# Performance work log

Measured on AMD Instinct MI355X. Metric: run time of the kernel, lower is better.

## Reference

```python
import jax, jax.numpy as jnp
import numpy as np
import math

N = 100000
D = 128       # input_dim
DK = 32       # d_k
H = 4         # heads
DV = D // H   # d_v = 32
DFF = 512     # 4 * input_dim
EPS = 1e-5


def layer_norm(x, g, b):
    mu = jnp.mean(x, axis=-1, keepdims=True)
    var = jnp.var(x, axis=-1, keepdims=True)
    return (x - mu) * jax.lax.rsqrt(var + EPS) * g + b


def setup_inputs() -> dict:
    key = jax.random.key(0)
    ks = jax.random.split(key, 10)
    x = jax.random.normal(ks[0], (N, D), dtype=jnp.float32)
    neighbor_index = jax.random.randint(ks[1], (N, 4), 0, N)
    # xavier-ish scaled params
    w_q = jax.random.normal(ks[2], (H, D, DK), dtype=jnp.float32) * math.sqrt(2.0 / (D + DK))
    w_k = jax.random.normal(ks[3], (H, 5, D, DK), dtype=jnp.float32) * math.sqrt(2.0 / (D + DK))
    w_v = jax.random.normal(ks[4], (H, 5, D, DV), dtype=jnp.float32) * math.sqrt(2.0 / (D + DV))
    W1 = jax.random.normal(ks[5], (D, DFF), dtype=jnp.float32) * math.sqrt(1.0 / D)
    b1 = jnp.zeros((DFF,), dtype=jnp.float32)
    W2 = jax.random.normal(ks[6], (DFF, D), dtype=jnp.float32) * math.sqrt(1.0 / DFF)
    b2 = jnp.zeros((D,), dtype=jnp.float32)
    g1 = jnp.ones((D,), dtype=jnp.float32)
    beta1 = jnp.zeros((D,), dtype=jnp.float32)
    g2 = jnp.ones((D,), dtype=jnp.float32)
    beta2 = jnp.zeros((D,), dtype=jnp.float32)
    return {"x": x, "neighbor_index": neighbor_index, "w_q": w_q, "w_k": w_k,
            "w_v": w_v, "W1": W1, "b1": b1, "W2": W2, "b2": b2,
            "g1": g1, "beta1": beta1, "g2": g2, "beta2": beta2}


def attention(x, neighbor_index, w_q, w_k, w_v):
    # gather the 4 typed neighbors and prepend the self node -> (N, 5, D)
    x_nb = jnp.concatenate([x[:, None, :], x[neighbor_index]], axis=1)
    Q = jnp.einsum('nd,hdk->hnk', x, w_q)                 # (H, N, DK)
    K = jnp.einsum('nrd,hrdk->hnrk', x_nb, w_k)           # (H, N, 5, DK)
    V = jnp.einsum('nrd,hrdv->hnrv', x_nb, w_v)           # (H, N, 5, DV)
    A = jnp.einsum('hnk,hnrk->hnr', Q, K) / math.sqrt(DK)
    # NOTE: original torch code applies softmax over dim=1 (the node axis),
    # reproduced faithfully here.
    A = jax.nn.softmax(A, axis=1)
    Z = jnp.einsum('hnr,hnrv->hnv', A, V)                 # (H, N, DV)
    return jnp.transpose(Z, (1, 0, 2)).reshape(x.shape[0], -1)  # (N, H*DV)


def reference(x, neighbor_index, w_q, w_k, w_v, W1, b1, W2, b2, g1, beta1, g2, beta2):
    attn = attention(x, neighbor_index, w_q, w_k, w_v)
    h = layer_norm(x + attn, g1, beta1)
    ffn = jax.nn.relu(h @ W1 + b1) @ W2 + b2
    return layer_norm(h + ffn, g2, beta2)
```

## Files before the change

kernel.cpp:

```cpp
#include <hip/hip_runtime.h>
#include <hip/hip_bf16.h>

typedef unsigned short u16;
typedef __attribute__((ext_vector_type(8))) short short8;
typedef __attribute__((ext_vector_type(4))) float f32x4;
typedef __attribute__((ext_vector_type(4))) float float4v;
typedef __attribute__((ext_vector_type(4))) unsigned short us4;
typedef __attribute__((ext_vector_type(2))) unsigned int uint2v;

#define NN       100000
#define OFF_WK   16384
#define OFF_WV   98304
#define OFF_W1   180224
#define PACK_ELEMS 311296

#define WS_LWS   0u
#define WS_PM    8000000u
#define WS_PS    8000640u
#define WS_MHR   8001280u
#define WS_ISHR  8001408u
#define WS_PK    8001536u
#define WS_XB    8624128u
#define WS_SV    34224128u

#define PWS_PITCH 36
#define PWS_SLICE 1280

static __device__ __forceinline__ float b2f(u16 u){
  unsigned int i = ((unsigned int)u) << 16;
  float f; __builtin_memcpy(&f, &i, 4); return f;
}
static __device__ __forceinline__ u16 f2b(float f){
  unsigned int i; __builtin_memcpy(&i, &f, 4);
  i += 0x7FFFu + ((i >> 16) & 1u);
  return (u16)(i >> 16);
}
static __device__ __forceinline__ f32x4 mfma16(short8 a, short8 b, f32x4 c){
  return __builtin_amdgcn_mfma_f32_16x16x32_bf16(a, b, c, 0, 0, 0);
}
static __device__ __forceinline__ bool detect32(const void* g1){
  return ((const u16*)g1)[0] == 0;
}
static __device__ __forceinline__ float ldf(const void* p, size_t i, bool is32){
  return is32 ? ((const float*)p)[i] : b2f(((const u16*)p)[i]);
}
static __device__ __forceinline__ short8 lds_afrag(const u16* p){
  uint2v a = *(const uint2v*)p;
  uint2v b = *(const uint2v*)(p + 4);
  short8 r;
  unsigned int* rp = (unsigned int*)&r;
  rp[0] = a.x; rp[1] = a.y; rp[2] = b.x; rp[3] = b.y;
  return r;
}

__global__ __launch_bounds__(256) void k_convert_x(
    const void* __restrict__ x, const void* __restrict__ g1, u16* __restrict__ xb)
{
  const bool is32 = detect32(g1);
  size_t i = (size_t)blockIdx.x * 256 + threadIdx.x;
  us4 o;
  if (is32){
    float4v v = ((const float4v*)x)[i];
    o.x = f2b(v.x); o.y = f2b(v.y); o.z = f2b(v.z); o.w = f2b(v.w);
  } else {
    o = ((const us4*)x)[i];
  }
  ((us4*)xb)[i] = o;
}

__global__ __launch_bounds__(256) void k_convert_small(
    const void* b1, const void* b2, const void* g1, const void* be1,
    const void* g2, const void* be2, u16* __restrict__ sv)
{
  const bool is32 = detect32(g1);
  for (int i = threadIdx.x; i < 1152; i += 256){
    const void* src; int off;
    if      (i < 512) { src = b1;  off = i; }
    else if (i < 640) { src = b2;  off = i - 512; }
    else if (i < 768) { src = g1;  off = i - 640; }
    else if (i < 896) { src = be1; off = i - 768; }
    else if (i < 1024){ src = g2;  off = i - 896; }
    else              { src = be2; off = i - 1024; }
    sv[i] = f2b(ldf(src, off, is32));
  }
}

__global__ __launch_bounds__(256) void k_pack(
    const void* __restrict__ wq, const void* __restrict__ wk,
    const void* __restrict__ wv, const void* __restrict__ W1,
    const void* __restrict__ W2, const void* __restrict__ g1,
    u16* __restrict__ pk)
{
  const bool is32 = detect32(g1);
  int p = blockIdx.x * 256 + threadIdx.x;
  if (p >= PACK_ELEMS) return;
  float v;
  if (p < OFF_WK){
    int q = p;
    int j = q & 7, lane = (q >> 3) & 63, tk = q >> 9;
    int kb = tk & 3, t = tk >> 2;
    int kd = kb*32 + (lane>>4)*8 + j, nc = t*16 + (lane & 15);
    v = ldf(wq, (size_t)(nc>>5)*4096 + kd*32 + (nc & 31), is32);
  } else if (p < OFF_WV){
    int q = p - OFF_WK; int r = q >> 14; q &= 16383;
    int j = q & 7, lane = (q >> 3) & 63, tk = q >> 9;
    int kb = tk & 3, t = tk >> 2;
    int kd = kb*32 + (lane>>4)*8 + j, nc = t*16 + (lane & 15);
    v = ldf(wk, (size_t)((nc>>5)*5 + r)*4096 + kd*32 + (nc & 31), is32);
  } else if (p < OFF_W1){
    int q = p - OFF_WV; int r = q >> 14; q &= 16383;
    int j = q & 7, lane = (q >> 3) & 63, tk = q >> 9;
    int kb = tk & 3, t = tk >> 2;
    int kd = kb*32 + (lane>>4)*8 + j, nc = t*16 + (lane & 15);
    v = ldf(wv, (size_t)((nc>>5)*5 + r)*4096 + kd*32 + (nc & 31), is32);
  } else {
    int q = p - OFF_W1;
    int j = q & 7, lane = (q >> 3) & 63, rest = q >> 9;
    int pairIdx = rest >> 4, sub = rest & 15;
    int c = pairIdx >> 2, kb2 = pairIdx & 3;
    int half = lane >> 4, mc = lane & 15;
    if (sub < 8){
      int u = sub >> 2, kb = sub & 3;
      int kd = kb*32 + half*8 + j;
      int nc = c*128 + (kb2*2+u)*16 + mc;
      v = ldf(W1, (size_t)kd*512 + nc, is32);
    } else {
      int t = sub - 8;
      int kd = (c*4+kb2)*32 + half*8 + j;
      int nc = t*16 + mc;
      v = ldf(W2, (size_t)kd*128 + nc, is32);
    }
  }
  pk[p] = f2b(v);
}

__global__ __launch_bounds__(256, 3) void k_qk(
    const u16* __restrict__ x, const int* __restrict__ nbr,
    const u16* __restrict__ pw, float* __restrict__ lws)
{
  __shared__ __align__(16) u16 sbuf[16384];
  const int tid = threadIdx.x, lane = tid & 63, wv = tid >> 6;
  const int m = lane & 15, quad = lane >> 4;
  const int n0 = blockIdx.x * 128 + wv * 32;
  const bool act0 = (n0 < NN), act1 = (n0 + 16 < NN);

  const short8* sb8 = (const short8*)sbuf;
  for (int s = tid; s < 2048; s += 256)
    ((short8*)sbuf)[s] = ((const short8*)pw)[s];
  __syncthreads();

  short8 a[2][4];
  f32x4 q[2][8];
  #pragma unroll
  for (int tl = 0; tl < 2; tl++)
    #pragma unroll
    for (int t = 0; t < 8; t++) q[tl][t] = (f32x4){0.f,0.f,0.f,0.f};

  #pragma unroll
  for (int tl = 0; tl < 2; tl++){
    if (!(tl ? act1 : act0)) continue;
    const short8* xp = (const short8*)(x + (size_t)(n0 + tl*16 + m) * 128);
    #pragma unroll
    for (int kb = 0; kb < 4; kb++) a[tl][kb] = xp[kb*4 + quad];
  }
  #pragma unroll
  for (int t = 0; t < 8; t++){
    short8 bfr[4];
    #pragma unroll
    for (int kb = 0; kb < 4; kb++) bfr[kb] = sb8[(t*4+kb)*64 + lane];
    #pragma unroll
    for (int tl = 0; tl < 2; tl++){
      if (!(tl ? act1 : act0)) continue;
      #pragma unroll
      for (int kb = 0; kb < 4; kb++) q[tl][t] = mfma16(a[tl][kb], bfr[kb], q[tl][t]);
    }
  }

  for (int r = 0; r < 5; r++){
    __syncthreads();
    for (int s = tid; s < 2048; s += 256)
      ((short8*)sbuf)[s] = ((const short8*)(pw + OFF_WK + (size_t)r*16384))[s];
    __syncthreads();
    if (r > 0){
      #pragma unroll
      for (int tl = 0; tl < 2; tl++){
        if (!(tl ? act1 : act0)) continue;
        int node = nbr[(size_t)(n0 + tl*16 + m)*4 + (r-1)];
        const short8* xp = (const short8*)(x + (size_t)node * 128);
        #pragma unroll
        for (int kb = 0; kb < 4; kb++) a[tl][kb] = xp[kb*4 + quad];
      }
    }
    #pragma unroll
    for (int h = 0; h < 4; h++){
      short8 b0[4], b1f[4];
      #pragma unroll
      for (int kb = 0; kb < 4; kb++){
        b0[kb]  = sb8[((2*h  )*4+kb)*64 + lane];
        b1f[kb] = sb8[((2*h+1)*4+kb)*64 + lane];
      }
      #pragma unroll
      for (int tl = 0; tl < 2; tl++){
        if (!(tl ? act1 : act0)) continue;
        f32x4 k0 = {0.f,0.f,0.f,0.f}, k1 = {0.f,0.f,0.f,0.f};
        #pragma unroll
        for (int kb = 0; kb < 4; kb++){
          k0 = mfma16(a[tl][kb], b0[kb],  k0);
          k1 = mfma16(a[tl][kb], b1f[kb], k1);
        }
        float p[4];
        #pragma unroll
        for (int i = 0; i < 4; i++) p[i] = q[tl][2*h][i]*k0[i] + q[tl][2*h+1][i]*k1[i];
        #pragma unroll
        for (int mask = 1; mask < 16; mask <<= 1){
          #pragma unroll
          for (int i = 0; i < 4; i++) p[i] += __shfl_xor(p[i], mask, 16);
        }
        if (m == 0){
          #pragma unroll
          for (int i = 0; i < 4; i++)
            lws[(size_t)(h*5+r)*NN + n0 + tl*16 + quad*4 + i]
                = p[i] * 0.17677669529663687f;
        }
      }
    }
  }
}

__global__ __launch_bounds__(256) void k_red_part(
    const float* __restrict__ lws, float* __restrict__ pm, float* __restrict__ ps)
{
  const int hr = blockIdx.x >> 3, pb = blockIdx.x & 7;
  const int start = pb * 12500, end = start + 12500;
  const float* v = lws + (size_t)hr * NN;
  __shared__ float red[256];
  float mx = -1e30f;
  for (int i = start + threadIdx.x; i < end; i += 256) mx = fmaxf(mx, v[i]);
  red[threadIdx.x] = mx; __syncthreads();
  for (int s = 128; s > 0; s >>= 1){
    if ((int)threadIdx.x < s) red[threadIdx.x] = fmaxf(red[threadIdx.x], red[threadIdx.x+s]);
    __syncthreads();
  }
  mx = red[0]; __syncthreads();
  float sm = 0.f;
  for (int i = start + threadIdx.x; i < end; i += 256) sm += __expf(v[i] - mx);
  red[threadIdx.x] = sm; __syncthreads();
  for (int s = 128; s > 0; s >>= 1){
    if ((int)threadIdx.x < s) red[threadIdx.x] += red[threadIdx.x+s];
    __syncthreads();
  }
  if (threadIdx.x == 0){ pm[blockIdx.x] = mx; ps[blockIdx.x] = red[0]; }
}

__global__ __launch_bounds__(64) void k_red_fin(
    const float* __restrict__ pm, const float* __restrict__ ps,
    float* __restrict__ mhr, float* __restrict__ ishr)
{
  int t = threadIdx.x;
  if (t < 20){
    float M = -1e30f;
    for (int b = 0; b < 8; b++) M = fmaxf(M, pm[t*8+b]);
    float S = 0.f;
    for (int b = 0; b < 8; b++) S += ps[t*8+b] * __expf(pm[t*8+b] - M);
    mhr[t] = M; ishr[t] = 1.0f / S;
  }
}

__global__ __launch_bounds__(256, 3) void k_attn_ffn(
    const u16* __restrict__ x, const void* __restrict__ xraw,
    const int* __restrict__ nbr,
    const u16* __restrict__ pw, const float* __restrict__ lws,
    const float* __restrict__ mhr, const float* __restrict__ ishr,
    const u16* __restrict__ sv, const void* __restrict__ g1raw,
    float* __restrict__ out)
{
  __shared__ __align__(16) u16 sbuf[16384];
  __shared__ __align__(16) u16 upool[5120];
  const int tid = threadIdx.x, lane = tid & 63, wv = tid >> 6;
  const int m = lane & 15, quad = lane >> 4;
  const int n0 = blockIdx.x * 128 + wv * 32;
  const bool act0 = (n0 < NN), act1 = (n0 + 16 < NN);
  const bool is32 = detect32(g1raw);
  const u16* b1s = sv;
  const u16* b2s = sv + 512;
  const u16* g1s = sv + 640;
  const u16* be1s = sv + 768;
  const u16* g2s = sv + 896;
  const u16* be2s = sv + 1024;
  const short8* sb8 = (const short8*)sbuf;
  float* attw_w = ((float*)upool) + wv * 640;
  u16*   pws_w  = upool + wv * PWS_SLICE;

  for (int j = lane; j < 640; j += 64){
    int tl = j / 320, rem = j - tl*320;
    int r = rem >> 6, h = (rem >> 4) & 3, mm = rem & 15, hr = h*5 + r;
    int node = n0 + tl*16 + mm;
    attw_w[j] = (node < NN)
        ? __expf(lws[(size_t)hr*NN + node] - mhr[hr]) * ishr[hr] : 0.f;
  }

  f32x4 zacc[2][8];
  #pragma unroll
  for (int tl = 0; tl < 2; tl++)
    #pragma unroll
    for (int t = 0; t < 8; t++) zacc[tl][t] = (f32x4){0.f,0.f,0.f,0.f};

  short8 a2[2][4];
  for (int r = 0; r < 5; r++){
    __syncthreads();
    for (int s = tid; s < 2048; s += 256)
      ((short8*)sbuf)[s] = ((const short8*)(pw + OFF_WV + (size_t)r*16384))[s];
    __syncthreads();

    #pragma unroll
    for (int tl = 0; tl < 2; tl++){
      if (!(tl ? act1 : act0)) continue;
      int rowb = n0 + tl*16;
      const short8* xp;
      if (r == 0) xp = (const short8*)(x + (size_t)(rowb + m) * 128);
      else {
        int node = nbr[(size_t)(rowb + m)*4 + (r-1)];
        xp = (const short8*)(x + (size_t)node * 128);
      }
      #pragma unroll
      for (int kb = 0; kb < 4; kb++) a2[tl][kb] = xp[kb*4 + quad];
    }
    #pragma unroll
    for (int t = 0; t < 8; t++){
      short8 bfr[4];
      #pragma unroll
      for (int kb = 0; kb < 4; kb++) bfr[kb] = sb8[(t*4+kb)*64 + lane];
      int h = t >> 1;
      #pragma unroll
      for (int tl = 0; tl < 2; tl++){
        if (!(tl ? act1 : act0)) continue;
        f32x4 v = {0.f,0.f,0.f,0.f};
        #pragma unroll
        for (int kb = 0; kb < 4; kb++) v = mfma16(a2[tl][kb], bfr[kb], v);
        const float* aw = attw_w + tl*320 + (r*4+h)*16;
        #pragma unroll
        for (int i = 0; i < 4; i++) zacc[tl][t][i] += aw[quad*4+i] * v[i];
      }
    }
  }

  float mu[2][4], rs[2][4];
  #pragma unroll
  for (int tl = 0; tl < 2; tl++){
    if (!(tl ? act1 : act0)) continue;
    int rowb = n0 + tl*16;
    #pragma unroll
    for (int t = 0; t < 8; t++)
      #pragma unroll
      for (int i = 0; i < 4; i++)
        zacc[tl][t][i] += ldf(xraw, (size_t)(rowb + quad*4 + i)*128 + t*16 + m, is32);
    float s1[4] = {0,0,0,0}, s2[4] = {0,0,0,0};
    #pragma unroll
    for (int t = 0; t < 8; t++)
      #pragma unroll
      for (int i = 0; i < 4; i++){ float y = zacc[tl][t][i]; s1[i] += y; s2[i] += y*y; }
    #pragma unroll
    for (int mask = 1; mask < 16; mask <<= 1){
      #pragma unroll
      for (int i = 0; i < 4; i++){
        s1[i] += __shfl_xor(s1[i], mask, 16);
        s2[i] += __shfl_xor(s2[i], mask, 16);
      }
    }
    #pragma unroll
    for (int i = 0; i < 4; i++){
      mu[tl][i] = s1[i] * (1.f/128.f);
      float var = s2[i] * (1.f/128.f) - mu[tl][i]*mu[tl][i];
      rs[tl][i] = rsqrtf(var + 1e-5f);
    }
  }

  unsigned int hDp[2][8][2];
  short8 ah[2][4];
  #pragma unroll
  for (int kb = 0; kb < 4; kb++){
    #pragma unroll
    for (int u = 0; u < 2; u++){
      int t = kb*2 + u;
      #pragma unroll
      for (int tl = 0; tl < 2; tl++){
        if (!(tl ? act1 : act0)) continue;
        float gg = b2f(g1s[t*16+m]), bb = b2f(be1s[t*16+m]);
        u16 hv[4];
        #pragma unroll
        for (int i = 0; i < 4; i++){
          hv[i] = f2b((zacc[tl][t][i]-mu[tl][i])*rs[tl][i]*gg + bb);
          pws_w[(tl*16 + quad*4 + i)*PWS_PITCH + u*16 + m] = hv[i];
        }
        hDp[tl][t][0] = (unsigned int)hv[0] | ((unsigned int)hv[1] << 16);
        hDp[tl][t][1] = (unsigned int)hv[2] | ((unsigned int)hv[3] << 16);
      }
    }
    #pragma unroll
    for (int tl = 0; tl < 2; tl++)
      ah[tl][kb] = lds_afrag(pws_w + (tl*16 + m)*PWS_PITCH + quad*8);
  }

  f32x4 f2acc[2][8];
  #pragma unroll
  for (int tl = 0; tl < 2; tl++)
    #pragma unroll
    for (int t = 0; t < 8; t++) f2acc[tl][t] = (f32x4){0.f,0.f,0.f,0.f};

  for (int c = 0; c < 4; c++){
    for (int kp = 0; kp < 2; kp++){
      __syncthreads();
      for (int s = tid; s < 2048; s += 256)
        ((short8*)sbuf)[s] =
            ((const short8*)(pw + OFF_W1 + (size_t)(c*4 + kp*2)*8192))[s];
      __syncthreads();
      #pragma unroll
      for (int kb2w = 0; kb2w < 2; kb2w++){
        int kb2 = kp*2 + kb2w;
        const short8* w1f = sb8 + kb2w*1024;
        const short8* w2f = w1f + 512;
        #pragma unroll
        for (int u = 0; u < 2; u++){
          short8 bfr[4];
          #pragma unroll
          for (int kb = 0; kb < 4; kb++) bfr[kb] = w1f[(u*4+kb)*64 + lane];
          float b1c = b2f(b1s[c*128 + (kb2*2+u)*16 + m]);
          #pragma unroll
          for (int tl = 0; tl < 2; tl++){
            if (!(tl ? act1 : act0)) continue;
            f32x4 g = {0.f,0.f,0.f,0.f};
            #pragma unroll
            for (int kb = 0; kb < 4; kb++) g = mfma16(ah[tl][kb], bfr[kb], g);
            #pragma unroll
            for (int i = 0; i < 4; i++)
              pws_w[(tl*16 + quad*4 + i)*PWS_PITCH + u*16 + m]
                  = f2b(fmaxf(g[i] + b1c, 0.f));
          }
        }
        short8 ag[2];
        #pragma unroll
        for (int tl = 0; tl < 2; tl++)
          ag[tl] = lds_afrag(pws_w + (tl*16 + m)*PWS_PITCH + quad*8);
        #pragma unroll
        for (int t = 0; t < 8; t++){
          short8 bf = w2f[t*64 + lane];
          #pragma unroll
          for (int tl = 0; tl < 2; tl++){
            if (!(tl ? act1 : act0)) continue;
            f2acc[tl][t] = mfma16(ag[tl], bf, f2acc[tl][t]);
          }
        }
      }
    }
  }

  #pragma unroll
  for (int tl = 0; tl < 2; tl++){
    if (!(tl ? act1 : act0)) continue;
    int rowb = n0 + tl*16;
    #pragma unroll
    for (int t = 0; t < 8; t++){
      float b2c = b2f(b2s[t*16 + m]);
      f2acc[tl][t][0] += b2f((u16)(hDp[tl][t][0] & 0xffff)) + b2c;
      f2acc[tl][t][1] += b2f((u16)(hDp[tl][t][0] >> 16))    + b2c;
      f2acc[tl][t][2] += b2f((u16)(hDp[tl][t][1] & 0xffff)) + b2c;
      f2acc[tl][t][3] += b2f((u16)(hDp[tl][t][1] >> 16))    + b2c;
    }
    float s1[4] = {0,0,0,0}, s2[4] = {0,0,0,0};
    #pragma unroll
    for (int t = 0; t < 8; t++)
      #pragma unroll
      for (int i = 0; i < 4; i++){ float y = f2acc[tl][t][i]; s1[i] += y; s2[i] += y*y; }
    #pragma unroll
    for (int mask = 1; mask < 16; mask <<= 1){
      #pragma unroll
      for (int i = 0; i < 4; i++){
        s1[i] += __shfl_xor(s1[i], mask, 16);
        s2[i] += __shfl_xor(s2[i], mask, 16);
      }
    }
    float mu2[4], rs2[4];
    #pragma unroll
    for (int i = 0; i < 4; i++){
      mu2[i] = s1[i] * (1.f/128.f);
      float var = s2[i] * (1.f/128.f) - mu2[i]*mu2[i];
      rs2[i] = rsqrtf(var + 1e-5f);
    }
    #pragma unroll
    for (int t = 0; t < 8; t++){
      float gg = b2f(g2s[t*16+m]), bb = b2f(be2s[t*16+m]);
      #pragma unroll
      for (int i = 0; i < 4; i++)
        out[(size_t)(rowb + quad*4 + i)*128 + t*16 + m] =
            (f2acc[tl][t][i]-mu2[i])*rs2[i]*gg + bb;
    }
  }
}

extern "C" void kernel_launch(void* const* d_in, const int* in_sizes, int n_in,
                              void* d_out, int out_size, void* d_ws, size_t ws_size,
                              hipStream_t stream)
{
  const void* x   = d_in[0];
  const int*  nbr = (const int*)d_in[1];
  const void* wq  = d_in[2];
  const void* wk  = d_in[3];
  const void* wv  = d_in[4];
  const void* W1  = d_in[5];
  const void* b1  = d_in[6];
  const void* W2  = d_in[7];
  const void* b2  = d_in[8];
  const void* g1  = d_in[9];
  const void* be1 = d_in[10];
  const void* g2  = d_in[11];
  const void* be2 = d_in[12];
  float* out = (float*)d_out;

  char* ws = (char*)d_ws;
  float* lws  = (float*)(ws + WS_LWS);
  float* pm   = (float*)(ws + WS_PM);
  float* ps   = (float*)(ws + WS_PS);
  float* mhr  = (float*)(ws + WS_MHR);
  float* ishr = (float*)(ws + WS_ISHR);
  u16*   pk   = (u16*)  (ws + WS_PK);
  u16*   xb   = (u16*)  (ws + WS_XB);
  u16*   sv   = (u16*)  (ws + WS_SV);

  k_convert_x<<<dim3(12500), dim3(256), 0, stream>>>(x, g1, xb);
  k_convert_small<<<dim3(1), dim3(256), 0, stream>>>(b1, b2, g1, be1, g2, be2, sv);
  k_pack<<<dim3((PACK_ELEMS+255)/256), dim3(256), 0, stream>>>(wq, wk, wv, W1, W2, g1, pk);
  k_qk<<<dim3((NN+127)/128), dim3(256), 0, stream>>>(xb, nbr, pk, lws);
  k_red_part<<<dim3(160), dim3(256), 0, stream>>>(lws, pm, ps);
  k_red_fin<<<dim3(1), dim3(64), 0, stream>>>(pm, ps, mhr, ishr);
  k_attn_ffn<<<dim3((NN+127)/128), dim3(256), 0, stream>>>(xb, x, nbr, pk, lws, mhr, ishr,
                                                           sv, g1, out);
}
```

Before: 353.1 us.

## Double-buffer weight tiles in LDS with register prefetch and gather prefetch

Both main kernels now stage weight tiles through a double-buffered LDS area. The next tile and the next neighbor-row gather are loaded into registers while the current tile's MFMAs run, which cuts the two barriers per stage down to one and hides global load latency. Neighbor indices are fetched once as a vector load, and the LDS pitch becomes 40 so A-fragments can be read with a single 16-byte load. The cost is twice the LDS and extra registers, so occupancy falls from 3 to 2 blocks per CU.

```diff
diff --git a/kernel.cpp b/kernel.cpp
--- a/kernel.cpp
+++ b/kernel.cpp
@@ -6,7 +6,7 @@
 typedef __attribute__((ext_vector_type(4))) float f32x4;
 typedef __attribute__((ext_vector_type(4))) float float4v;
 typedef __attribute__((ext_vector_type(4))) unsigned short us4;
-typedef __attribute__((ext_vector_type(2))) unsigned int uint2v;
+typedef __attribute__((ext_vector_type(4))) int int4v;
 
 #define NN       100000
 #define OFF_WK   16384
@@ -23,7 +23,7 @@
 #define WS_XB    8624128u
 #define WS_SV    34224128u
 
-#define PWS_PITCH 36
+#define PWS_PITCH 40
 #define PWS_SLICE 1280
 
 static __device__ __forceinline__ float b2f(u16 u){
@@ -43,14 +43,6 @@
 }
 static __device__ __forceinline__ float ldf(const void* p, size_t i, bool is32){
   return is32 ? ((const float*)p)[i] : b2f(((const u16*)p)[i]);
-}
-static __device__ __forceinline__ short8 lds_afrag(const u16* p){
-  uint2v a = *(const uint2v*)p;
-  uint2v b = *(const uint2v*)(p + 4);
-  short8 r;
-  unsigned int* rp = (unsigned int*)&r;
-  rp[0] = a.x; rp[1] = a.y; rp[2] = b.x; rp[3] = b.y;
-  return r;
 }
 
 __global__ __launch_bounds__(256) void k_convert_x(
@@ -134,61 +126,75 @@
   pk[p] = f2b(v);
 }
 
-__global__ __launch_bounds__(256, 3) void k_qk(
+__global__ __launch_bounds__(256, 2) void k_qk(
     const u16* __restrict__ x, const int* __restrict__ nbr,
     const u16* __restrict__ pw, float* __restrict__ lws)
 {
-  __shared__ __align__(16) u16 sbuf[16384];
+  __shared__ __align__(16) u16 sbuf[32768];
   const int tid = threadIdx.x, lane = tid & 63, wv = tid >> 6;
   const int m = lane & 15, quad = lane >> 4;
   const int n0 = blockIdx.x * 128 + wv * 32;
   const bool act0 = (n0 < NN), act1 = (n0 + 16 < NN);
-
-  const short8* sb8 = (const short8*)sbuf;
-  for (int s = tid; s < 2048; s += 256)
-    ((short8*)sbuf)[s] = ((const short8*)pw)[s];
-  __syncthreads();
-
-  short8 a[2][4];
-  f32x4 q[2][8];
-  #pragma unroll
-  for (int tl = 0; tl < 2; tl++)
-    #pragma unroll
-    for (int t = 0; t < 8; t++) q[tl][t] = (f32x4){0.f,0.f,0.f,0.f};
-
+  short8* sb = (short8*)sbuf;
+  const short8* wq8 = (const short8*)pw;
+  const short8* wk8 = (const short8*)(pw + OFF_WK);
+
+  int nd[2][4];
+  short8 a2[2][4], a2n[2][4];
   #pragma unroll
   for (int tl = 0; tl < 2; tl++){
     if (!(tl ? act1 : act0)) continue;
+    int4v t4 = *(const int4v*)(nbr + (size_t)(n0 + tl*16 + m)*4);
+    nd[tl][0]=t4.x; nd[tl][1]=t4.y; nd[tl][2]=t4.z; nd[tl][3]=t4.w;
     const short8* xp = (const short8*)(x + (size_t)(n0 + tl*16 + m) * 128);
     #pragma unroll
-    for (int kb = 0; kb < 4; kb++) a[tl][kb] = xp[kb*4 + quad];
-  }
+    for (int kb = 0; kb < 4; kb++) a2[tl][kb] = xp[kb*4 + quad];
+  }
+
+  short8 wreg[8];
+  #pragma unroll
+  for (int k = 0; k < 8; k++) wreg[k] = wq8[tid + k*256];
+  #pragma unroll
+  for (int k = 0; k < 8; k++) sb[tid + k*256] = wreg[k];
+  __syncthreads();
+
+  #pragma unroll
+  for (int k = 0; k < 8; k++) wreg[k] = wk8[tid + k*256];
+  f32x4 q[2][8];
+  #pragma unroll
+  for (int tl = 0; tl < 2; tl++)
+    #pragma unroll
+    for (int t = 0; t < 8; t++) q[tl][t] = (f32x4){0.f,0.f,0.f,0.f};
   #pragma unroll
   for (int t = 0; t < 8; t++){
     short8 bfr[4];
     #pragma unroll
-    for (int kb = 0; kb < 4; kb++) bfr[kb] = sb8[(t*4+kb)*64 + lane];
+    for (int kb = 0; kb < 4; kb++) bfr[kb] = sb[(t*4+kb)*64 + lane];
     #pragma unroll
     for (int tl = 0; tl < 2; tl++){
       if (!(tl ? act1 : act0)) continue;
       #pragma unroll
-      for (int kb = 0; kb < 4; kb++) q[tl][t] = mfma16(a[tl][kb], bfr[kb], q[tl][t]);
-    }
-  }
+      for (int kb = 0; kb < 4; kb++) q[tl][t] = mfma16(a2[tl][kb], bfr[kb], q[tl][t]);
+    }
+  }
+  {
+    short8* nxt = (short8*)(sbuf + 16384);
+    #pragma unroll
+    for (int k = 0; k < 8; k++) nxt[tid + k*256] = wreg[k];
+  }
+  __syncthreads();
 
   for (int r = 0; r < 5; r++){
-    __syncthreads();
-    for (int s = tid; s < 2048; s += 256)
-      ((short8*)sbuf)[s] = ((const short8*)(pw + OFF_WK + (size_t)r*16384))[s];
-    __syncthreads();
-    if (r > 0){
+    const short8* cur = (const short8*)(sbuf + ((r+1)&1)*16384);
+    if (r < 4){
+      #pragma unroll
+      for (int k = 0; k < 8; k++) wreg[k] = wk8[(r+1)*2048 + tid + k*256];
       #pragma unroll
       for (int tl = 0; tl < 2; tl++){
         if (!(tl ? act1 : act0)) continue;
-        int node = nbr[(size_t)(n0 + tl*16 + m)*4 + (r-1)];
-        const short8* xp = (const short8*)(x + (size_t)node * 128);
-        #pragma unroll
-        for (int kb = 0; kb < 4; kb++) a[tl][kb] = xp[kb*4 + quad];
+        const short8* gp = (const short8*)(x + (size_t)nd[tl][r] * 128);
+        #pragma unroll
+        for (int kb = 0; kb < 4; kb++) a2n[tl][kb] = gp[kb*4 + quad];
       }
     }
     #pragma unroll
@@ -196,8 +202,8 @@
       short8 b0[4], b1f[4];
       #pragma unroll
       for (int kb = 0; kb < 4; kb++){
-        b0[kb]  = sb8[((2*h  )*4+kb)*64 + lane];
-        b1f[kb] = sb8[((2*h+1)*4+kb)*64 + lane];
+        b0[kb]  = cur[((2*h  )*4+kb)*64 + lane];
+        b1f[kb] = cur[((2*h+1)*4+kb)*64 + lane];
       }
       #pragma unroll
       for (int tl = 0; tl < 2; tl++){
@@ -205,8 +211,8 @@
         f32x4 k0 = {0.f,0.f,0.f,0.f}, k1 = {0.f,0.f,0.f,0.f};
         #pragma unroll
         for (int kb = 0; kb < 4; kb++){
-          k0 = mfma16(a[tl][kb], b0[kb],  k0);
-          k1 = mfma16(a[tl][kb], b1f[kb], k1);
+          k0 = mfma16(a2[tl][kb], b0[kb],  k0);
+          k1 = mfma16(a2[tl][kb], b1f[kb], k1);
         }
         float p[4];
         #pragma unroll
@@ -224,6 +230,16 @@
         }
       }
     }
+    if (r < 4){
+      short8* nxt = (short8*)(sbuf + (r&1)*16384);
+      #pragma unroll
+      for (int k = 0; k < 8; k++) nxt[tid + k*256] = wreg[k];
+      #pragma unroll
+      for (int tl = 0; tl < 2; tl++)
+        #pragma unroll
+        for (int kb = 0; kb < 4; kb++) a2[tl][kb] = a2n[tl][kb];
+    }
+    __syncthreads();
   }
 }
 
@@ -266,7 +282,7 @@
   }
 }
 
-__global__ __launch_bounds__(256, 3) void k_attn_ffn(
+__global__ __launch_bounds__(256, 2) void k_attn_ffn(
     const u16* __restrict__ x, const void* __restrict__ xraw,
     const int* __restrict__ nbr,
     const u16* __restrict__ pw, const float* __restrict__ lws,
@@ -274,7 +290,7 @@
     const u16* __restrict__ sv, const void* __restrict__ g1raw,
     float* __restrict__ out)
 {
-  __shared__ __align__(16) u16 sbuf[16384];
+  __shared__ __align__(16) u16 sbuf[32768];
   __shared__ __align__(16) u16 upool[5120];
   const int tid = threadIdx.x, lane = tid & 63, wv = tid >> 6;
   const int m = lane & 15, quad = lane >> 4;
@@ -287,7 +303,9 @@
   const u16* be1s = sv + 768;
   const u16* g2s = sv + 896;
   const u16* be2s = sv + 1024;
-  const short8* sb8 = (const short8*)sbuf;
+  short8* sb = (short8*)sbuf;
+  const short8* wv8 = (const short8*)(pw + OFF_WV);
+  const short8* wf8 = (const short8*)(pw + OFF_W1);
   float* attw_w = ((float*)upool) + wv * 640;
   u16*   pws_w  = upool + wv * PWS_SLICE;
 
@@ -299,37 +317,49 @@
         ? __expf(lws[(size_t)hr*NN + node] - mhr[hr]) * ishr[hr] : 0.f;
   }
 
+  int nd[2][4];
+  short8 a2[2][4], a2n[2][4];
+  #pragma unroll
+  for (int tl = 0; tl < 2; tl++){
+    if (!(tl ? act1 : act0)) continue;
+    int4v t4 = *(const int4v*)(nbr + (size_t)(n0 + tl*16 + m)*4);
+    nd[tl][0]=t4.x; nd[tl][1]=t4.y; nd[tl][2]=t4.z; nd[tl][3]=t4.w;
+    const short8* xp = (const short8*)(x + (size_t)(n0 + tl*16 + m) * 128);
+    #pragma unroll
+    for (int kb = 0; kb < 4; kb++) a2[tl][kb] = xp[kb*4 + quad];
+  }
+
+  short8 wreg[8];
+  #pragma unroll
+  for (int k = 0; k < 8; k++) wreg[k] = wv8[tid + k*256];
+  #pragma unroll
+  for (int k = 0; k < 8; k++) sb[tid + k*256] = wreg[k];
+  __syncthreads();
+
   f32x4 zacc[2][8];
   #pragma unroll
   for (int tl = 0; tl < 2; tl++)
     #pragma unroll
     for (int t = 0; t < 8; t++) zacc[tl][t] = (f32x4){0.f,0.f,0.f,0.f};
 
-  short8 a2[2][4];
   for (int r = 0; r < 5; r++){
-    __syncthreads();
-    for (int s = tid; s < 2048; s += 256)
-      ((short8*)sbuf)[s] = ((const short8*)(pw + OFF_WV + (size_t)r*16384))[s];
-    __syncthreads();
-
-    #pragma unroll
-    for (int tl = 0; tl < 2; tl++){
-      if (!(tl ? act1 : act0)) continue;
-      int rowb = n0 + tl*16;
-      const short8* xp;
-      if (r == 0) xp = (const short8*)(x + (size_t)(rowb + m) * 128);
-      else {
-        int node = nbr[(size_t)(rowb + m)*4 + (r-1)];
-        xp = (const short8*)(x + (size_t)node * 128);
-      }
-      #pragma unroll
-      for (int kb = 0; kb < 4; kb++) a2[tl][kb] = xp[kb*4 + quad];
+    const short8* cur = (const short8*)(sbuf + (r&1)*16384);
+    if (r < 4){
+      #pragma unroll
+      for (int k = 0; k < 8; k++) wreg[k] = wv8[(r+1)*2048 + tid + k*256];
+      #pragma unroll
+      for (int tl = 0; tl < 2; tl++){
+        if (!(tl ? act1 : act0)) continue;
+        const short8* gp = (const short8*)(x + (size_t)nd[tl][r] * 128);
+        #pragma unroll
+        for (int kb = 0; kb < 4; kb++) a2n[tl][kb] = gp[kb*4 + quad];
+      }
     }
     #pragma unroll
     for (int t = 0; t < 8; t++){
       short8 bfr[4];
       #pragma unroll
-      for (int kb = 0; kb < 4; kb++) bfr[kb] = sb8[(t*4+kb)*64 + lane];
+      for (int kb = 0; kb < 4; kb++) bfr[kb] = cur[(t*4+kb)*64 + lane];
       int h = t >> 1;
       #pragma unroll
       for (int tl = 0; tl < 2; tl++){
@@ -342,7 +372,20 @@
         for (int i = 0; i < 4; i++) zacc[tl][t][i] += aw[quad*4+i] * v[i];
       }
     }
-  }
+    if (r < 4){
+      short8* nxt = (short8*)(sbuf + ((r+1)&1)*16384);
+      #pragma unroll
+      for (int k = 0; k < 8; k++) nxt[tid + k*256] = wreg[k];
+      #pragma unroll
+      for (int tl = 0; tl < 2; tl++)
+        #pragma unroll
+        for (int kb = 0; kb < 4; kb++) a2[tl][kb] = a2n[tl][kb];
+    }
+    __syncthreads();
+  }
+
+  #pragma unroll
+  for (int k = 0; k < 8; k++) wreg[k] = wf8[tid + k*256];
 
   float mu[2][4], rs[2][4];
   #pragma unroll
@@ -398,8 +441,12 @@
     }
     #pragma unroll
     for (int tl = 0; tl < 2; tl++)
-      ah[tl][kb] = lds_afrag(pws_w + (tl*16 + m)*PWS_PITCH + quad*8);
-  }
+      ah[tl][kb] = *(const short8*)(pws_w + (tl*16 + m)*PWS_PITCH + quad*8);
+  }
+
+  #pragma unroll
+  for (int k = 0; k < 8; k++) sb[tid + k*256] = wreg[k];
+  __syncthreads();
 
   f32x4 f2acc[2][8];
   #pragma unroll
@@ -407,51 +454,56 @@
     #pragma unroll
     for (int t = 0; t < 8; t++) f2acc[tl][t] = (f32x4){0.f,0.f,0.f,0.f};
 
-  for (int c = 0; c < 4; c++){
-    for (int kp = 0; kp < 2; kp++){
-      __syncthreads();
-      for (int s = tid; s < 2048; s += 256)
-        ((short8*)sbuf)[s] =
-            ((const short8*)(pw + OFF_W1 + (size_t)(c*4 + kp*2)*8192))[s];
-      __syncthreads();
-      #pragma unroll
-      for (int kb2w = 0; kb2w < 2; kb2w++){
-        int kb2 = kp*2 + kb2w;
-        const short8* w1f = sb8 + kb2w*1024;
-        const short8* w2f = w1f + 512;
-        #pragma unroll
-        for (int u = 0; u < 2; u++){
-          short8 bfr[4];
+  for (int s = 0; s < 8; s++){
+    const short8* cur = (const short8*)(sbuf + (s&1)*16384);
+    const int c = s >> 1, kp = s & 1;
+    if (s < 7){
+      #pragma unroll
+      for (int k = 0; k < 8; k++) wreg[k] = wf8[(s+1)*2048 + tid + k*256];
+    }
+    #pragma unroll
+    for (int kb2w = 0; kb2w < 2; kb2w++){
+      int kb2 = kp*2 + kb2w;
+      const short8* w1f = cur + kb2w*1024;
+      const short8* w2f = w1f + 512;
+      #pragma unroll
+      for (int u = 0; u < 2; u++){
+        short8 bfr[4];
+        #pragma unroll
+        for (int kb = 0; kb < 4; kb++) bfr[kb] = w1f[(u*4+kb)*64 + lane];
+        float b1c = b2f(b1s[c*128 + (kb2*2+u)*16 + m]);
+        #pragma unroll
+        for (int tl = 0; tl < 2; tl++){
+          if (!(tl ? act1 : act0)) continue;
+          f32x4 g = {0.f,0.f,0.f,0.f};
           #pragma unroll
-          for (int kb = 0; kb < 4; kb++) bfr[kb] = w1f[(u*4+kb)*64 + lane];
-          float b1c = b2f(b1s[c*128 + (kb2*2+u)*16 + m]);
+          for (int kb = 0; kb < 4; kb++) g = mfma16(ah[tl][kb], bfr[kb], g);
           #pragma unroll
-          for (int tl = 0; tl < 2; tl++){
-            if (!(tl ? act1 : act0)) continue;
-            f32x4 g = {0.f,0.f,0.f,0.f};
-            #pragma unroll
-            for (int kb = 0; kb < 4; kb++) g = mfma16(ah[tl][kb], bfr[kb], g);
-            #pragma unroll
-            for (int i = 0; i < 4; i++)
-              pws_w[(tl*16 + quad*4 + i)*PWS_PITCH + u*16 + m]
-                  = f2b(fmaxf(g[i] + b1c, 0.f));
-          }
+          for (int i = 0; i < 4; i++)
+            pws_w[(tl*16 + quad*4 + i)*PWS_PITCH + u*16 + m]
+                = f2b(fmaxf(g[i] + b1c, 0.f));
         }
-        short8 ag[2];
-        #pragma unroll
-        for (int tl = 0; tl < 2; tl++)
-          ag[tl] = lds_afrag(pws_w + (tl*16 + m)*PWS_PITCH + quad*8);
-        #pragma unroll
-        for (int t = 0; t < 8; t++){
-          short8 bf = w2f[t*64 + lane];
-          #pragma unroll
-          for (int tl = 0; tl < 2; tl++){
-            if (!(tl ? act1 : act0)) continue;
-            f2acc[tl][t] = mfma16(ag[tl], bf, f2acc[tl][t]);
-          }
+      }
+      short8 ag[2];
+      #pragma unroll
+      for (int tl = 0; tl < 2; tl++)
+        ag[tl] = *(const short8*)(pws_w + (tl*16 + m)*PWS_PITCH + quad*8);
+      #pragma unroll
+      for (int t = 0; t < 8; t++){
+        short8 bf = w2f[t*64 + lane];
+        #pragma unroll
+        for (int tl = 0; tl < 2; tl++){
+          if (!(tl ? act1 : act0)) continue;
+          f2acc[tl][t] = mfma16(ag[tl], bf, f2acc[tl][t]);
         }
       }
     }
+    if (s < 7){
+      short8* nxt = (short8*)(sbuf + ((s+1)&1)*16384);
+      #pragma unroll
+      for (int k = 0; k < 8; k++) nxt[tid + k*256] = wreg[k];
+    }
+    __syncthreads();
   }
 
   #pragma unroll
```

Result: faster. 302.7 us (-14.3%).
